# Performance work log

Measured on AMD Instinct MI355X. Metric: run time of the kernel, lower is better.

The kernel has to match this reference:

```python
import jax, jax.numpy as jnp
import numpy as np

NUM_HEADS = 8

def setup_inputs() -> dict:
    key = jax.random.key(0)
    ks = jax.random.split(key, 9)
    B, C, H, W = 2, 256, 64, 64
    s = 0.02  # weight init scale
    return {
        "x": jax.random.normal(ks[0], (B, C, H, W), dtype=jnp.float32),
        "Wq": jax.random.normal(ks[1], (C, C), dtype=jnp.float32) * s,
        "bq": jnp.zeros((C,), dtype=jnp.float32),
        "Wk": jax.random.normal(ks[2], (C, C), dtype=jnp.float32) * s,
        "bk": jnp.zeros((C,), dtype=jnp.float32),
        "Wv": jax.random.normal(ks[3], (C, C), dtype=jnp.float32) * s,
        "bv": jnp.zeros((C,), dtype=jnp.float32),
        "Wo": jax.random.normal(ks[4], (C, C), dtype=jnp.float32) * s,
        "bo": jnp.zeros((C,), dtype=jnp.float32),
    }

def _conv1x1(x, W, b):
    # 1x1 Conv2d == channel-mixing GEMM: [out_c,in_c] x [B,in_c,H,W]
    return jnp.einsum('oc,bchw->bohw', W, x) + b[None, :, None, None]

def reference(x, Wq, bq, Wk, bk, Wv, bv, Wo, bo):
    B, C, H, W = x.shape
    h = NUM_HEADS
    d = C // h
    N = H * W
    scale = d ** (-0.5)
    q = _conv1x1(x, Wq, bq).reshape(B, h, d, N)
    k = _conv1x1(x, Wk, bk).reshape(B, h, d, N)
    v = _conv1x1(x, Wv, bv).reshape(B, h, d, N)
    attn = jnp.einsum('bhdk,bhdm->bhkm', q, k) * scale  # [B,h,N,N]
    attn = jax.nn.softmax(attn, axis=-1)
    # dropout p=0.0 / eval mode -> identity
    out = jnp.einsum('bhkm,bhdm->bhdk', attn, v)  # [B,h,d,N]
    out = out.reshape(B, C, H, W)
    return x + _conv1x1(out, Wo, bo)
```

## Files before the change

kernel.cpp:

```cpp
#include <hip/hip_runtime.h>

#define B_    2
#define C_    256
#define NH    8
#define HD    32
#define N_    4096
#define SCALE_LOG2E 0.25503485f

typedef float f32x4 __attribute__((ext_vector_type(4)));
typedef short bf16x8 __attribute__((ext_vector_type(8)));

#define MFMA16(a, b, c) __builtin_amdgcn_mfma_f32_16x16x32_bf16(a, b, c, 0, 0, 0)

__device__ __forceinline__ unsigned short f2bf(float f) {
    unsigned int u = __float_as_uint(f);
    u += 0x7fffu + ((u >> 16) & 1u);
    return (unsigned short)(u >> 16);
}

__global__ __launch_bounds__(256) void wconv_kernel(
    const float* __restrict__ Wq, const float* __restrict__ Wk,
    const float* __restrict__ Wv, const float* __restrict__ Wo,
    unsigned short* __restrict__ Wbf)
{
    const int m = blockIdx.y;
    const float* src = (m == 0) ? Wq : (m == 1) ? Wk : (m == 2) ? Wv : Wo;
    const int i = (blockIdx.x * 256 + threadIdx.x) * 4;
    float4 v = *reinterpret_cast<const float4*>(&src[i]);
    unsigned int d0 = (unsigned)f2bf(v.x) | ((unsigned)f2bf(v.y) << 16);
    unsigned int d1 = (unsigned)f2bf(v.z) | ((unsigned)f2bf(v.w) << 16);
    *reinterpret_cast<uint2*>(&Wbf[(size_t)m * 65536 + i]) = make_uint2(d0, d1);
}

__global__ __launch_bounds__(256) void proj_kernel(
    const float* __restrict__ x,
    const unsigned short* __restrict__ Wbf,
    const float* __restrict__ bq, const float* __restrict__ bk,
    const float* __restrict__ bv,
    unsigned short* __restrict__ Qt, unsigned short* __restrict__ Kt,
    unsigned short* __restrict__ Vn)
{
    const int n0 = blockIdx.x * 64;
    const int b  = blockIdx.y;
    const int pr = blockIdx.z;
    const unsigned short* W = Wbf + (size_t)pr * 65536;
    const float* bias = (pr == 0) ? bq : (pr == 1) ? bk : bv;

    __shared__ __align__(16) unsigned short XT[64][264];

    const int t = threadIdx.x;
    #pragma unroll
    for (int s = 0; s < 16; ++s) {
        const int ic = s * 16 + (t >> 4);
        const int nn = (t & 15) * 4;
        float4 v = *reinterpret_cast<const float4*>(&x[((size_t)b * C_ + ic) * N_ + n0 + nn]);
        XT[nn + 0][ic] = f2bf(v.x);
        XT[nn + 1][ic] = f2bf(v.y);
        XT[nn + 2][ic] = f2bf(v.z);
        XT[nn + 3][ic] = f2bf(v.w);
    }
    __syncthreads();

    const int wave = t >> 6, lane = t & 63;
    const int l15 = lane & 15, l4 = lane >> 4;
    const int oc0 = wave * 64;

    f32x4 acc[4][4];
    #pragma unroll
    for (int i = 0; i < 4; ++i)
        #pragma unroll
        for (int j = 0; j < 4; ++j)
            acc[i][j] = (f32x4){0.f, 0.f, 0.f, 0.f};

    #pragma unroll
    for (int kc = 0; kc < 8; ++kc) {
        bf16x8 a[4];
        #pragma unroll
        for (int mi = 0; mi < 4; ++mi)
            a[mi] = *reinterpret_cast<const bf16x8*>(&XT[mi * 16 + l15][kc * 32 + l4 * 8]);
        #pragma unroll
        for (int oci = 0; oci < 4; ++oci) {
            bf16x8 bf = *reinterpret_cast<const bf16x8*>(
                &W[(size_t)(oc0 + oci * 16 + l15) * C_ + kc * 32 + l4 * 8]);
            #pragma unroll
            for (int mi = 0; mi < 4; ++mi)
                acc[mi][oci] = MFMA16(a[mi], bf, acc[mi][oci]);
        }
    }

    const float mult = (pr == 0) ? SCALE_LOG2E : 1.0f;
    #pragma unroll
    for (int oci = 0; oci < 4; ++oci) {
        const int oc = oc0 + oci * 16 + l15;
        const float bb = bias[oc];
        const int h = oc >> 5, d = oc & 31;
        #pragma unroll
        for (int mi = 0; mi < 4; ++mi) {
            #pragma unroll
            for (int r = 0; r < 4; ++r) {
                const int n = n0 + mi * 16 + l4 * 4 + r;
                const unsigned short bfv = f2bf((acc[mi][oci][r] + bb) * mult);
                if (pr == 2)
                    Vn[(((size_t)b * NH + h) * HD + d) * N_ + n] = bfv;
                else if (pr == 0)
                    Qt[(((size_t)b * NH + h) * N_ + n) * HD + d] = bfv;
                else
                    Kt[(((size_t)b * NH + h) * N_ + n) * HD + d] = bfv;
            }
        }
    }
}

__global__ __launch_bounds__(256) void attn_kernel(
    const unsigned short* __restrict__ Qt,
    const unsigned short* __restrict__ Kt,
    const unsigned short* __restrict__ Vn,
    unsigned short* __restrict__ AO)
{
    const int b = blockIdx.z, h = blockIdx.y;
    const int t = threadIdx.x, wave = t >> 6, lane = t & 63;
    const int l15 = lane & 15, l4 = lane >> 4;
    const size_t bh = (size_t)b * NH + h;
    const int qw0 = blockIdx.x * 64 + wave * 16;

    const unsigned short* Qb = Qt + bh * (size_t)N_ * HD;
    const unsigned short* Kb = Kt + bh * (size_t)N_ * HD;
    const unsigned short* Vb = Vn + bh * (size_t)HD * N_;

    __shared__ __align__(16) unsigned short Klds[64][40];
    __shared__ __align__(16) unsigned short Vlds[32][72];
    __shared__ __align__(16) unsigned short Plds[4][16][72];
    unsigned short (*Pw)[72] = Plds[wave];

    const bf16x8 qa = *reinterpret_cast<const bf16x8*>(
        &Qb[(size_t)(qw0 + l15) * HD + l4 * 8]);

    f32x4 o[2];
    o[0] = (f32x4){0.f, 0.f, 0.f, 0.f};
    o[1] = (f32x4){0.f, 0.f, 0.f, 0.f};
    float ls = 0.f;
    const f32x4 zero = (f32x4){0.f, 0.f, 0.f, 0.f};

    for (int kt = 0; kt < N_ / 64; ++kt) {
        {
            const int kr = t >> 2, kcol = (t & 3) * 8;
            *reinterpret_cast<int4*>(&Klds[kr][kcol]) =
                *reinterpret_cast<const int4*>(&Kb[(size_t)(kt * 64 + kr) * HD + kcol]);
            const int vr = t >> 3, vc = (t & 7) * 8;
            *reinterpret_cast<int4*>(&Vlds[vr][vc]) =
                *reinterpret_cast<const int4*>(&Vb[(size_t)vr * N_ + kt * 64 + vc]);
        }
        __syncthreads();

        #pragma unroll
        for (int kf = 0; kf < 4; ++kf) {
            bf16x8 kb = *reinterpret_cast<const bf16x8*>(&Klds[kf * 16 + l15][l4 * 8]);
            f32x4 s = MFMA16(kb, qa, zero);
            float p0 = exp2f(s[0]), p1 = exp2f(s[1]);
            float p2 = exp2f(s[2]), p3 = exp2f(s[3]);
            ls += (p0 + p1) + (p2 + p3);
            unsigned int d0, d1;
            asm("v_cvt_pk_bf16_f32 %0, %1, %2" : "=v"(d0) : "v"(p0), "v"(p1));
            asm("v_cvt_pk_bf16_f32 %0, %1, %2" : "=v"(d1) : "v"(p2), "v"(p3));
            *reinterpret_cast<uint2*>(&Pw[l15][kf * 16 + l4 * 4]) = make_uint2(d0, d1);
        }

        #pragma unroll
        for (int k32 = 0; k32 < 2; ++k32) {
            bf16x8 pa = *reinterpret_cast<const bf16x8*>(&Pw[l15][k32 * 32 + l4 * 8]);
            #pragma unroll
            for (int df = 0; df < 2; ++df) {
                bf16x8 vb = *reinterpret_cast<const bf16x8*>(
                    &Vlds[df * 16 + l15][k32 * 32 + l4 * 8]);
                o[df] = MFMA16(pa, vb, o[df]);
            }
        }
        __syncthreads();
    }

    ls += __shfl_xor(ls, 16, 64);
    ls += __shfl_xor(ls, 32, 64);

    #pragma unroll
    for (int r = 0; r < 4; ++r) {
        const float invr = 1.0f / __shfl(ls, l4 * 4 + r, 64);
        const int q = qw0 + l4 * 4 + r;
        #pragma unroll
        for (int df = 0; df < 2; ++df)
            AO[(bh * (size_t)N_ + q) * HD + df * 16 + l15] = f2bf(o[df][r] * invr);
    }
}

__global__ __launch_bounds__(256) void oproj_kernel(
    const float* __restrict__ x,
    const unsigned short* __restrict__ Wob, const float* __restrict__ bo,
    const unsigned short* __restrict__ AO,
    float* __restrict__ out)
{
    const int b = blockIdx.y;
    const int n0 = blockIdx.x * 32;
    const int t = threadIdx.x, wave = t >> 6, lane = t & 63;
    const int l15 = lane & 15, l4 = lane >> 4;
    const int oc0 = wave * 64;

    f32x4 acc[4][2];
    #pragma unroll
    for (int i = 0; i < 4; ++i)
        #pragma unroll
        for (int j = 0; j < 2; ++j)
            acc[i][j] = (f32x4){0.f, 0.f, 0.f, 0.f};

    #pragma unroll
    for (int kc = 0; kc < 8; ++kc) {
        bf16x8 bfr[2];
        #pragma unroll
        for (int nf = 0; nf < 2; ++nf)
            bfr[nf] = *reinterpret_cast<const bf16x8*>(
                &AO[(((size_t)b * NH + kc) * N_ + n0 + nf * 16 + l15) * HD + l4 * 8]);
        #pragma unroll
        for (int ocf = 0; ocf < 4; ++ocf) {
            bf16x8 a = *reinterpret_cast<const bf16x8*>(
                &Wob[(size_t)(oc0 + ocf * 16 + l15) * C_ + kc * 32 + l4 * 8]);
            #pragma unroll
            for (int nf = 0; nf < 2; ++nf)
                acc[ocf][nf] = MFMA16(a, bfr[nf], acc[ocf][nf]);
        }
    }

    #pragma unroll
    for (int ocf = 0; ocf < 4; ++ocf)
        #pragma unroll
        for (int r = 0; r < 4; ++r) {
            const int oc = oc0 + ocf * 16 + l4 * 4 + r;
            const float bb = bo[oc];
            #pragma unroll
            for (int nf = 0; nf < 2; ++nf) {
                const size_t idx = ((size_t)b * C_ + oc) * (size_t)N_ + n0 + nf * 16 + l15;
                out[idx] = x[idx] + bb + acc[ocf][nf][r];
            }
        }
}

extern "C" void kernel_launch(void* const* d_in, const int* in_sizes, int n_in,
                              void* d_out, int out_size, void* d_ws, size_t ws_size,
                              hipStream_t stream)
{
    const float* x  = (const float*)d_in[0];
    const float* Wq = (const float*)d_in[1];
    const float* bq = (const float*)d_in[2];
    const float* Wk = (const float*)d_in[3];
    const float* bk = (const float*)d_in[4];
    const float* Wv = (const float*)d_in[5];
    const float* bv = (const float*)d_in[6];
    const float* Wo = (const float*)d_in[7];
    const float* bo = (const float*)d_in[8];

    const size_t buf = (size_t)B_ * NH * N_ * HD;
    unsigned short* Qt  = (unsigned short*)d_ws;
    unsigned short* Kt  = Qt + buf;
    unsigned short* Vn  = Kt + buf;
    unsigned short* AO  = Vn + buf;
    unsigned short* Wbf = AO + buf;

    wconv_kernel<<<dim3(64, 4), 256, 0, stream>>>(Wq, Wk, Wv, Wo, Wbf);
    proj_kernel<<<dim3(N_ / 64, B_, 3), 256, 0, stream>>>(
        x, Wbf, bq, bk, bv, Qt, Kt, Vn);
    attn_kernel<<<dim3(N_ / 64, NH, B_), 256, 0, stream>>>(Qt, Kt, Vn, AO);
    oproj_kernel<<<dim3(N_ / 32, B_), 256, 0, stream>>>(
        x, Wbf + 3 * 65536, bo, AO, (float*)d_out);
}
```

Before: 216.3 us.

## Rewrite attention inner loop with 32x32 MFMA and register-resident probabilities

The attention kernel moves from 16x16x32 to 32x32x16 bf16 MFMA, with each wave covering 32 queries and each block 128. The P tile now stays in registers, rearranged with v_permlane32_swap, so it no longer round-trips through LDS. K and V LDS tiles use an XOR swizzle instead of padding to avoid bank conflicts, and exp2 uses the hardware instruction directly. This cuts LDS traffic and instruction count per key tile and doubles K/V reuse per block. In exchange the grid has half as many blocks and each thread holds more registers, and the bf16 fragment layout and output mapping are harder to verify.

Measured after the change: 187.3 us. 13.4% less time.

```diff
diff --git a/kernel.cpp b/kernel.cpp
--- a/kernel.cpp
+++ b/kernel.cpp
@@ -7,15 +7,25 @@
 #define N_    4096
 #define SCALE_LOG2E 0.25503485f
 
-typedef float f32x4 __attribute__((ext_vector_type(4)));
+typedef float f32x4  __attribute__((ext_vector_type(4)));
+typedef float f32x16 __attribute__((ext_vector_type(16)));
 typedef short bf16x8 __attribute__((ext_vector_type(8)));
 
 #define MFMA16(a, b, c) __builtin_amdgcn_mfma_f32_16x16x32_bf16(a, b, c, 0, 0, 0)
+#define MFMA32(a, b, c) __builtin_amdgcn_mfma_f32_32x32x16_bf16(a, b, c, 0, 0, 0)
 
 __device__ __forceinline__ unsigned short f2bf(float f) {
     unsigned int u = __float_as_uint(f);
     u += 0x7fffu + ((u >> 16) & 1u);
     return (unsigned short)(u >> 16);
+}
+
+__device__ __forceinline__ float fast_exp2(float x) {
+#if __has_builtin(__builtin_amdgcn_exp2f)
+    return __builtin_amdgcn_exp2f(x);
+#else
+    float r; asm("v_exp_f32 %0, %1" : "=v"(r) : "v"(x)); return r;
+#endif
 }
 
 __global__ __launch_bounds__(256) void wconv_kernel(
@@ -119,75 +129,93 @@
 {
     const int b = blockIdx.z, h = blockIdx.y;
     const int t = threadIdx.x, wave = t >> 6, lane = t & 63;
-    const int l15 = lane & 15, l4 = lane >> 4;
+    const int l31 = lane & 31, hi = lane >> 5;
     const size_t bh = (size_t)b * NH + h;
-    const int qw0 = blockIdx.x * 64 + wave * 16;
+    const int qw0 = blockIdx.x * 128 + wave * 32;
 
     const unsigned short* Qb = Qt + bh * (size_t)N_ * HD;
     const unsigned short* Kb = Kt + bh * (size_t)N_ * HD;
     const unsigned short* Vb = Vn + bh * (size_t)HD * N_;
 
-    __shared__ __align__(16) unsigned short Klds[64][40];
-    __shared__ __align__(16) unsigned short Vlds[32][72];
-    __shared__ __align__(16) unsigned short Plds[4][16][72];
-    unsigned short (*Pw)[72] = Plds[wave];
-
-    const bf16x8 qa = *reinterpret_cast<const bf16x8*>(
-        &Qb[(size_t)(qw0 + l15) * HD + l4 * 8]);
-
-    f32x4 o[2];
-    o[0] = (f32x4){0.f, 0.f, 0.f, 0.f};
-    o[1] = (f32x4){0.f, 0.f, 0.f, 0.f};
+    __shared__ __align__(16) unsigned short Klds[64 * 32];
+    __shared__ __align__(16) unsigned short Vlds[32 * 64];
+
+    const bf16x8 q0 = *reinterpret_cast<const bf16x8*>(
+        &Qb[(size_t)(qw0 + l31) * HD + hi * 8]);
+    const bf16x8 q1 = *reinterpret_cast<const bf16x8*>(
+        &Qb[(size_t)(qw0 + l31) * HD + 16 + hi * 8]);
+
+    f32x16 o, zero16;
+    #pragma unroll
+    for (int j = 0; j < 16; ++j) { o[j] = 0.f; zero16[j] = 0.f; }
     float ls = 0.f;
-    const f32x4 zero = (f32x4){0.f, 0.f, 0.f, 0.f};
+
+    const int skr = t >> 2, skc = t & 3;
+    const int svd = t >> 3, svc = t & 7;
+    const int skoff = skr * 32 + ((skc ^ (skr & 3)) << 3);
+    const int svoff = svd * 64 + ((svc ^ (svd & 7)) << 3);
+
+    const int krow = l31 * 32;
+    const int kc0 = ((hi) ^ (l31 & 3)) << 3;
+    const int kc1 = ((2 + hi) ^ (l31 & 3)) << 3;
+    const int vrow = l31 * 64;
 
     for (int kt = 0; kt < N_ / 64; ++kt) {
-        {
-            const int kr = t >> 2, kcol = (t & 3) * 8;
-            *reinterpret_cast<int4*>(&Klds[kr][kcol]) =
-                *reinterpret_cast<const int4*>(&Kb[(size_t)(kt * 64 + kr) * HD + kcol]);
-            const int vr = t >> 3, vc = (t & 7) * 8;
-            *reinterpret_cast<int4*>(&Vlds[vr][vc]) =
-                *reinterpret_cast<const int4*>(&Vb[(size_t)vr * N_ + kt * 64 + vc]);
-        }
+        *reinterpret_cast<int4*>(&Klds[skoff]) =
+            *reinterpret_cast<const int4*>(&Kb[(size_t)(kt * 64 + skr) * HD + skc * 8]);
+        *reinterpret_cast<int4*>(&Vlds[svoff]) =
+            *reinterpret_cast<const int4*>(&Vb[(size_t)svd * N_ + kt * 64 + svc * 8]);
         __syncthreads();
 
         #pragma unroll
-        for (int kf = 0; kf < 4; ++kf) {
-            bf16x8 kb = *reinterpret_cast<const bf16x8*>(&Klds[kf * 16 + l15][l4 * 8]);
-            f32x4 s = MFMA16(kb, qa, zero);
-            float p0 = exp2f(s[0]), p1 = exp2f(s[1]);
-            float p2 = exp2f(s[2]), p3 = exp2f(s[3]);
-            ls += (p0 + p1) + (p2 + p3);
-            unsigned int d0, d1;
-            asm("v_cvt_pk_bf16_f32 %0, %1, %2" : "=v"(d0) : "v"(p0), "v"(p1));
-            asm("v_cvt_pk_bf16_f32 %0, %1, %2" : "=v"(d1) : "v"(p2), "v"(p3));
-            *reinterpret_cast<uint2*>(&Pw[l15][kf * 16 + l4 * 4]) = make_uint2(d0, d1);
-        }
-
-        #pragma unroll
-        for (int k32 = 0; k32 < 2; ++k32) {
-            bf16x8 pa = *reinterpret_cast<const bf16x8*>(&Pw[l15][k32 * 32 + l4 * 8]);
-            #pragma unroll
-            for (int df = 0; df < 2; ++df) {
-                bf16x8 vb = *reinterpret_cast<const bf16x8*>(
-                    &Vlds[df * 16 + l15][k32 * 32 + l4 * 8]);
-                o[df] = MFMA16(pa, vb, o[df]);
+        for (int ks = 0; ks < 2; ++ks) {
+            const int kbase = ks * 32 * 32;
+            bf16x8 a0 = *reinterpret_cast<const bf16x8*>(&Klds[kbase + krow + kc0]);
+            bf16x8 a1 = *reinterpret_cast<const bf16x8*>(&Klds[kbase + krow + kc1]);
+            f32x16 s = MFMA32(a0, q0, zero16);
+            s = MFMA32(a1, q1, s);
+
+            unsigned int w[8];
+            #pragma unroll
+            for (int j = 0; j < 8; ++j) {
+                float pa = fast_exp2(s[2 * j]);
+                float pb = fast_exp2(s[2 * j + 1]);
+                ls += pa + pb;
+                asm("v_cvt_pk_bf16_f32 %0, %1, %2" : "=v"(w[j]) : "v"(pa), "v"(pb));
             }
+            unsigned int x0 = w[0], y0 = w[2], x1 = w[1], y1 = w[3];
+            asm("v_permlane32_swap_b32 %0, %1" : "+v"(x0), "+v"(y0));
+            asm("v_permlane32_swap_b32 %0, %1" : "+v"(x1), "+v"(y1));
+            unsigned int x2 = w[4], y2 = w[6], x3 = w[5], y3 = w[7];
+            asm("v_permlane32_swap_b32 %0, %1" : "+v"(x2), "+v"(y2));
+            asm("v_permlane32_swap_b32 %0, %1" : "+v"(x3), "+v"(y3));
+            int4 pb0i = make_int4((int)x0, (int)x1, (int)y0, (int)y1);
+            int4 pb1i = make_int4((int)x2, (int)x3, (int)y2, (int)y3);
+            bf16x8 pfrag0 = *reinterpret_cast<bf16x8*>(&pb0i);
+            bf16x8 pfrag1 = *reinterpret_cast<bf16x8*>(&pb1i);
+
+            const int c0 = ((ks * 4 + hi) ^ (l31 & 7)) << 3;
+            const int c1 = ((ks * 4 + 2 + hi) ^ (l31 & 7)) << 3;
+            bf16x8 va = *reinterpret_cast<const bf16x8*>(&Vlds[vrow + c0]);
+            bf16x8 vb = *reinterpret_cast<const bf16x8*>(&Vlds[vrow + c1]);
+            o = MFMA32(va, pfrag0, o);
+            o = MFMA32(vb, pfrag1, o);
         }
         __syncthreads();
     }
 
-    ls += __shfl_xor(ls, 16, 64);
     ls += __shfl_xor(ls, 32, 64);
-
-    #pragma unroll
-    for (int r = 0; r < 4; ++r) {
-        const float invr = 1.0f / __shfl(ls, l4 * 4 + r, 64);
-        const int q = qw0 + l4 * 4 + r;
-        #pragma unroll
-        for (int df = 0; df < 2; ++df)
-            AO[(bh * (size_t)N_ + q) * HD + df * 16 + l15] = f2bf(o[df][r] * invr);
+    const float invr = 1.0f / ls;
+
+    #pragma unroll
+    for (int rr = 0; rr < 8; ++rr) {
+        const int r = rr * 2;
+        const int d = (r & 3) + 8 * (r >> 2) + 4 * hi;
+        float e0 = o[r] * invr, e1 = o[r + 1] * invr;
+        unsigned int pkv;
+        asm("v_cvt_pk_bf16_f32 %0, %1, %2" : "=v"(pkv) : "v"(e0), "v"(e1));
+        *reinterpret_cast<unsigned int*>(
+            &AO[(bh * (size_t)N_ + qw0 + l31) * HD + d]) = pkv;
     }
 }
 
@@ -265,7 +293,7 @@
     wconv_kernel<<<dim3(64, 4), 256, 0, stream>>>(Wq, Wk, Wv, Wo, Wbf);
     proj_kernel<<<dim3(N_ / 64, B_, 3), 256, 0, stream>>>(
         x, Wbf, bq, bk, bv, Qt, Kt, Vn);
-    attn_kernel<<<dim3(N_ / 64, NH, B_), 256, 0, stream>>>(Qt, Kt, Vn, AO);
+    attn_kernel<<<dim3(N_ / 128, NH, B_), 256, 0, stream>>>(Qt, Kt, Vn, AO);
     oproj_kernel<<<dim3(N_ / 32, B_), 256, 0, stream>>>(
         x, Wbf + 3 * 65536, bo, AO, (float*)d_out);
 }
```
